# Performance work log

Measured on AMD Instinct MI355X. Metric: run time of the kernel, lower is better.

Reference implementation:

```python
import jax, jax.numpy as jnp
import numpy as np

MAX_CACHE_LEN = 4096


def _rotate_half(t):
    d = t.shape[-1] // 2
    return jnp.concatenate([-t[..., d:], t[..., :d]], axis=-1)


def _apply_rope(t, cos, sin):
    # t: (B, S, H, D); cos/sin: (S, D)
    c = cos[None, :, None, :]
    s = sin[None, :, None, :]
    return t * c + _rotate_half(t) * s


def setup_inputs() -> dict:
    key = jax.random.key(0)
    ks = jax.random.split(key, 7)
    B, S, E, D, KVH = 1, 2048, 2048, 64, 8
    sc = 0.02
    x = jax.random.normal(ks[0], (B, S, E), dtype=jnp.float32)
    Wq = jax.random.normal(ks[1], (E, E), dtype=jnp.float32) * sc
    Wk = jax.random.normal(ks[2], (KVH * D, E), dtype=jnp.float32) * sc
    Wv = jax.random.normal(ks[3], (KVH * D, E), dtype=jnp.float32) * sc
    Wo = jax.random.normal(ks[4], (E, E), dtype=jnp.float32) * sc
    # RoPE tables
    pos = jnp.arange(S, dtype=jnp.float32)[:, None]
    inv_freq = 1.0 / (10000.0 ** (jnp.arange(0, D, 2, dtype=jnp.float32) / D))
    ang = pos * inv_freq[None, :]              # (S, D/2)
    ang = jnp.concatenate([ang, ang], axis=-1)  # (S, D)
    cos = jnp.cos(ang)
    sin = jnp.sin(ang)
    # additive causal mask (1,1,S,S): 0 where allowed, -1e9 where masked
    causal = jnp.tril(jnp.ones((S, S), dtype=bool))
    attn_mask = jnp.where(causal, 0.0, -1e9).astype(jnp.float32)[None, None]
    return {"x": x, "Wq": Wq, "Wk": Wk, "Wv": Wv, "Wo": Wo,
            "cos": cos, "sin": sin, "attn_mask": attn_mask, "last_pos": S}


def reference(x, Wq, Wk, Wv, Wo, cos, sin, attn_mask, last_pos):
    B, S, E = x.shape
    D = cos.shape[-1]
    H = E // D
    KVH = Wk.shape[0] // D
    group = H // KVH

    q = (x @ Wq.T).reshape(B, S, H, D)
    k = (x @ Wk.T).reshape(B, S, KVH, D)
    v = (x @ Wv.T).reshape(B, S, KVH, D)

    q = _apply_rope(q, cos, sin)
    k = _apply_rope(k, cos, sin)

    # KV-cache write (index_copy at positions [last_pos-S, last_pos)), then slice [:last_pos]
    key_cache = jnp.zeros((B, MAX_CACHE_LEN, KVH, D), dtype=x.dtype)
    value_cache = jnp.zeros((B, MAX_CACHE_LEN, KVH, D), dtype=x.dtype)
    key_cache = jax.lax.dynamic_update_slice(key_cache, jax.lax.stop_gradient(k), (0, last_pos - S, 0, 0))
    value_cache = jax.lax.dynamic_update_slice(value_cache, jax.lax.stop_gradient(v), (0, last_pos - S, 0, 0))
    kc = key_cache[:, :last_pos]    # (B, T, KVH, D)
    vc = value_cache[:, :last_pos]

    # GQA: repeat kv heads to match q heads
    kc = jnp.repeat(kc, group, axis=2)  # (B, T, H, D)
    vc = jnp.repeat(vc, group, axis=2)

    scale = 1.0 / np.sqrt(D)
    scores = jnp.einsum('bqhd,bkhd->bhqk', q, kc) * scale
    scores = scores + attn_mask
    probs = jax.nn.softmax(scores.astype(jnp.float32), axis=-1).astype(x.dtype)
    attn = jnp.einsum('bhqk,bkhd->bqhd', probs, vc)  # (B, S, H, D)
    out = attn.reshape(B, S, E) @ Wo.T
    return out
```

## Files before the change

### kernel.cpp

```cpp
#include <hip/hip_runtime.h>
#include <stdint.h>

typedef unsigned short u16;
typedef unsigned int   u32;

typedef __bf16 bf16x8 __attribute__((ext_vector_type(8)));
typedef float  fx4    __attribute__((ext_vector_type(4)));
typedef u16    u16x8  __attribute__((ext_vector_type(8)));
typedef u16    u16x4  __attribute__((ext_vector_type(4)));

typedef __attribute__((address_space(1))) unsigned int as1_u32;
typedef __attribute__((address_space(3))) unsigned int as3_u32;

__device__ __forceinline__ void gload_lds16(const void* g, void* lds) {
  __builtin_amdgcn_global_load_lds((const as1_u32*)(uintptr_t)g,
                                   (as3_u32*)(uintptr_t)lds, 16, 0, 0);
}

__device__ __forceinline__ float b2f(u32 bits) {
  union { u32 i; float f; } v; v.i = bits << 16; return v.f;
}
__device__ __forceinline__ u16 f2b(float f) {
  union { float f; u32 i; } v; v.f = f;
  u32 x = v.i;
  return (u16)((x + 0x7fffu + ((x >> 16) & 1u)) >> 16);
}
__device__ __forceinline__ u16 f2b_hw(float f) {
  union { __bf16 b; u16 u; } v; v.b = (__bf16)f; return v.u;
}

__global__ __launch_bounds__(256) void cast_kernel(
    const float* __restrict__ s0, const float* __restrict__ s1,
    const float* __restrict__ s2, const float* __restrict__ s3,
    const float* __restrict__ s4, u16* __restrict__ dst)
{
  const size_t i8 = ((size_t)blockIdx.x * 256 + threadIdx.x) * 8;
  if (i8 >= 14680064) return;
  const float* src; size_t off;
  if      (i8 <  4194304) { src = s0; off = i8; }
  else if (i8 <  8388608) { src = s1; off = i8 - 4194304; }
  else if (i8 <  9437184) { src = s2; off = i8 - 8388608; }
  else if (i8 < 10485760) { src = s3; off = i8 - 9437184; }
  else                    { src = s4; off = i8 - 10485760; }
  const float4 a = *(const float4*)(src + off);
  const float4 b = *(const float4*)(src + off + 4);
  u16x8 o;
  o[0] = f2b(a.x); o[1] = f2b(a.y); o[2] = f2b(a.z); o[3] = f2b(a.w);
  o[4] = f2b(b.x); o[5] = f2b(b.y); o[6] = f2b(b.z); o[7] = f2b(b.w);
  *(u16x8*)(dst + i8) = o;
}

template <int MODE>
__global__ __launch_bounds__(256) void gemm_bt(
    const u16* __restrict__ A, const u16* __restrict__ B0,
    const u16* __restrict__ B1, const u16* __restrict__ B2,
    void* __restrict__ Cv, int K, int split1, int split2, int ldc,
    const float* __restrict__ cosb, const float* __restrict__ sinb,
    u16* __restrict__ vtg)
{
  __shared__ __align__(16) u16 smem[4 * 8192];

  const int n0 = blockIdx.x * 128;
  const int m0 = blockIdx.y * 128;

  const u16* Bsel; int nb;
  if (n0 < split1)      { Bsel = B0; nb = n0; }
  else if (n0 < split2) { Bsel = B1; nb = n0 - split1; }
  else                  { Bsel = B2; nb = n0 - split2; }

  const int tid  = threadIdx.x;
  const int wave = tid >> 6, lane = tid & 63;
  const int wm = wave >> 1, wn = wave & 1;
  const int quad = lane >> 4, l16 = lane & 15;

  fx4 acc[4][4];
#pragma unroll
  for (int i = 0; i < 4; ++i)
#pragma unroll
    for (int j = 0; j < 4; ++j) acc[i][j] = fx4{0.f, 0.f, 0.f, 0.f};

  const int row = tid >> 2;
  const int cc  = (tid & 3) * 8;
  auto stage = [&](int kt) {
    u16* As = smem + (kt & 3) * 8192;
    u16* Bs = As + 4096;
    const int k0 = kt * 32;
#pragma unroll
    for (int i = 0; i < 2; ++i) {
      const int r2 = row + i * 64;
      const int s  = tid + i * 256;
      gload_lds16(A    + (size_t)(m0 + r2) * K + k0 + cc, As + s * 8);
      gload_lds16(Bsel + (size_t)(nb + r2) * K + k0 + cc, Bs + s * 8);
    }
  };

  const int KT = K >> 5;
  stage(0); stage(1); stage(2);

#pragma unroll 1
  for (int kt = 0; kt < KT; ++kt) {
    const int rem = KT - 1 - kt;
    if (rem >= 3)      asm volatile("s_waitcnt vmcnt(12)\n\ts_barrier" ::: "memory");
    else if (rem == 2) asm volatile("s_waitcnt vmcnt(8)\n\ts_barrier" ::: "memory");
    else if (rem == 1) asm volatile("s_waitcnt vmcnt(4)\n\ts_barrier" ::: "memory");
    else               asm volatile("s_waitcnt vmcnt(0)\n\ts_barrier" ::: "memory");
    if (kt + 3 < KT) stage(kt + 3);

    const u16* As = smem + (kt & 3) * 8192;
    const u16* Bs = As + 4096;

    bf16x8 af[4], bfr[4];
#pragma unroll
    for (int t = 0; t < 4; ++t) {
      af[t]  = *(const bf16x8*)&As[(wm * 64 + t * 16 + l16) * 32 + quad * 8];
      bfr[t] = *(const bf16x8*)&Bs[(wn * 64 + t * 16 + l16) * 32 + quad * 8];
    }
#pragma unroll
    for (int ti = 0; ti < 4; ++ti)
#pragma unroll
      for (int tj = 0; tj < 4; ++tj)
        acc[ti][tj] = __builtin_amdgcn_mfma_f32_16x16x32_bf16(
            af[ti], bfr[tj], acc[ti][tj], 0, 0, 0);
  }

  if (MODE == 1) {
    float* C = (float*)Cv;
#pragma unroll
    for (int ti = 0; ti < 4; ++ti) {
      const int row_b = m0 + wm * 64 + ti * 16 + quad * 4;
#pragma unroll
      for (int tj = 0; tj < 4; ++tj) {
        const int col = n0 + wn * 64 + tj * 16 + l16;
#pragma unroll
        for (int r = 0; r < 4; ++r)
          C[(size_t)(row_b + r) * ldc + col] = acc[ti][tj][r];
      }
    }
  } else {
    u16* C = (u16*)Cv;
    const int cb = n0 + wn * 64;
    if (cb < 2560) {
      const float qs = (cb < 2048) ? 0.125f : 1.0f;
#pragma unroll
      for (int ti = 0; ti < 4; ++ti) {
#pragma unroll
        for (int r = 0; r < 4; ++r) {
          const int s = m0 + wm * 64 + ti * 16 + quad * 4 + r;
          const float* cr = cosb + s * 64;
          const float* sr = sinb + s * 64;
          u16* orow = C + (size_t)s * 3072 + cb;
#pragma unroll
          for (int tj = 0; tj < 2; ++tj) {
            const int d0 = tj * 16 + l16, d1 = d0 + 32;
            const float x0 = acc[ti][tj][r], x1 = acc[ti][tj + 2][r];
            orow[d0] = f2b((x0 * cr[d0] - x1 * sr[d0]) * qs);
            orow[d1] = f2b((x1 * cr[d1] + x0 * sr[d1]) * qs);
          }
        }
      }
    } else {
      const int vr0 = cb - 2560;
#pragma unroll
      for (int ti = 0; ti < 4; ++ti) {
        const int s0 = m0 + wm * 64 + ti * 16 + quad * 4;
#pragma unroll
        for (int tj = 0; tj < 4; ++tj) {
          const int vr = vr0 + tj * 16 + l16;
          u16x4 o;
#pragma unroll
          for (int r = 0; r < 4; ++r) o[r] = f2b(acc[ti][tj][r]);
          *(u16x4*)(vtg + (size_t)vr * 2048 + s0) = o;
        }
      }
    }
  }
}

__global__ __launch_bounds__(256) void attn_kernel(
    const u16* __restrict__ qkv, const u16* __restrict__ vt,
    u16* __restrict__ attnbuf)
{
  const int h   = blockIdx.y;
  const int kvh = h >> 2;
  const int tid = threadIdx.x;
  const int w = tid >> 6, lane = tid & 63;
  const int quad = lane >> 4, l16 = lane & 15;

  __shared__ __align__(16) u16 Qs[64][72];
  __shared__ __align__(16) u16 Ks[128][72];
  __shared__ __align__(16) u16 Vh[2][64][72];
  __shared__ __align__(16) u16 Ps[4][16][72];

  const int kcol = 2048 + kvh * 64;

#pragma unroll 1
  for (int pass = 0; pass < 2; ++pass) {
    const int bx = pass ? (31 - blockIdx.x) : blockIdx.x;
    const int r0 = bx * 64;
    const int nhalf  = bx + 1;
    const int ntiles = (bx + 2) >> 1;

    __syncthreads();

#pragma unroll
    for (int i = 0; i < 2; ++i) {
      const int idx = tid + i * 256;
      const int r = idx >> 3, dc = (idx & 7) * 8;
      *(uint4*)&Qs[r][dc] =
          *(const uint4*)(qkv + (size_t)(r0 + r) * 3072 + h * 64 + dc);
    }

    fx4 O[4];
    float l_r[4];
#pragma unroll
    for (int c = 0; c < 4; ++c) O[c] = fx4{0.f, 0.f, 0.f, 0.f};
#pragma unroll
    for (int r = 0; r < 4; ++r) l_r[r] = 0.f;

#pragma unroll 1
    for (int kt = 0; kt < ntiles; ++kt) {
      const int k0 = kt * 128;
      __syncthreads();
#pragma unroll
      for (int i = 0; i < 4; ++i) {
        const int idx = tid + i * 256;
        const int j = idx >> 3, dc = (idx & 7) * 8;
        *(uint4*)&Ks[j][dc] =
            *(const uint4*)(qkv + (size_t)(k0 + j) * 3072 + kcol + dc);
      }
#pragma unroll
      for (int i = 0; i < 4; ++i) {
        const int idx = tid + i * 256;
        const int hh = idx >> 9, rem = idx & 511;
        const int j = rem >> 3, dc = (rem & 7) * 8;
        *(uint4*)&Vh[hh][j][dc] =
            *(const uint4*)(vt + (size_t)(kvh * 64 + j) * 2048 + k0 + hh * 64 + dc);
      }
      __syncthreads();

      const bf16x8 aq0 = *(const bf16x8*)&Qs[w * 16 + l16][quad * 8];
      const bf16x8 aq1 = *(const bf16x8*)&Qs[w * 16 + l16][32 + quad * 8];

#pragma unroll
      for (int hh = 0; hh < 2; ++hh) {
        const int half = kt * 2 + hh;
        if (half < nhalf) {
          const int k0h = k0 + hh * 64;

          fx4 sc[4];
#pragma unroll
          for (int c = 0; c < 4; ++c) {
            const bf16x8 b0 = *(const bf16x8*)&Ks[hh * 64 + c * 16 + l16][quad * 8];
            const bf16x8 b1 = *(const bf16x8*)&Ks[hh * 64 + c * 16 + l16][32 + quad * 8];
            fx4 z = fx4{0.f, 0.f, 0.f, 0.f};
            z     = __builtin_amdgcn_mfma_f32_16x16x32_bf16(aq0, b0, z, 0, 0, 0);
            sc[c] = __builtin_amdgcn_mfma_f32_16x16x32_bf16(aq1, b1, z, 0, 0, 0);
          }

          if (k0h >= r0) {
#pragma unroll
            for (int c = 0; c < 4; ++c)
#pragma unroll
              for (int r = 0; r < 4; ++r) {
                float p = __expf(sc[c][r]);
                if (k0h + c * 16 + l16 > r0 + w * 16 + quad * 4 + r) p = 0.f;
                l_r[r] += p;
                Ps[w][quad * 4 + r][c * 16 + l16] = f2b_hw(p);
              }
          } else {
#pragma unroll
            for (int c = 0; c < 4; ++c)
#pragma unroll
              for (int r = 0; r < 4; ++r) {
                const float p = __expf(sc[c][r]);
                l_r[r] += p;
                Ps[w][quad * 4 + r][c * 16 + l16] = f2b_hw(p);
              }
          }

          const bf16x8 ap0 = *(const bf16x8*)&Ps[w][l16][quad * 8];
          const bf16x8 ap1 = *(const bf16x8*)&Ps[w][l16][32 + quad * 8];
#pragma unroll
          for (int c = 0; c < 4; ++c) {
            const bf16x8 v0 = *(const bf16x8*)&Vh[hh][c * 16 + l16][quad * 8];
            const bf16x8 v1 = *(const bf16x8*)&Vh[hh][c * 16 + l16][32 + quad * 8];
            O[c] = __builtin_amdgcn_mfma_f32_16x16x32_bf16(ap0, v0, O[c], 0, 0, 0);
            O[c] = __builtin_amdgcn_mfma_f32_16x16x32_bf16(ap1, v1, O[c], 0, 0, 0);
          }
        }
      }
    }

#pragma unroll
    for (int r = 0; r < 4; ++r) {
      float l = l_r[r];
#pragma unroll
      for (int off = 1; off < 16; off <<= 1) l += __shfl_xor(l, off, 64);
      const float inv = 1.f / fmaxf(l, 1e-30f);
      const int qg = r0 + w * 16 + quad * 4 + r;
#pragma unroll
      for (int c = 0; c < 4; ++c)
        attnbuf[(size_t)qg * 2048 + h * 64 + c * 16 + l16] = f2b(O[c][r] * inv);
    }
  }
}

extern "C" void kernel_launch(void* const* d_in, const int* in_sizes, int n_in,
                              void* d_out, int out_size, void* d_ws, size_t ws_size,
                              hipStream_t stream) {
  const float* x    = (const float*)d_in[0];
  const float* Wq   = (const float*)d_in[1];
  const float* Wk   = (const float*)d_in[2];
  const float* Wv   = (const float*)d_in[3];
  const float* Wo   = (const float*)d_in[4];
  const float* cosb = (const float*)d_in[5];
  const float* sinb = (const float*)d_in[6];
  float* out = (float*)d_out;

  u16* ws      = (u16*)d_ws;
  u16* qkv     = ws;
  u16* attnbuf = ws + 6291456;
  u16* xb      = ws + 10485760;
  u16* Wqb     = ws + 14680064;
  u16* Wkb     = ws + 18874368;
  u16* Wvb     = ws + 19922944;
  u16* Wob     = ws + 20971520;
  u16* vtg     = ws + 25165824;

  cast_kernel<<<7168, 256, 0, stream>>>(x, Wq, Wk, Wv, Wo, xb);

  gemm_bt<0><<<dim3(24, 16), 256, 0, stream>>>(
      xb, Wqb, Wkb, Wvb, qkv, 2048, 2048, 2560, 3072, cosb, sinb, vtg);

  attn_kernel<<<dim3(16, 32), 256, 0, stream>>>(qkv, vtg, attnbuf);

  gemm_bt<1><<<dim3(16, 16), 256, 0, stream>>>(
      attnbuf, Wob, Wob, Wob, out, 2048, 1 << 30, 1 << 30, 2048, cosb, sinb, vtg);
}
```

Baseline: 230.6 us.

## Restructure attention into one query tile per block with double-buffered async KV loads

```diff
diff --git a/kernel.cpp b/kernel.cpp
--- a/kernel.cpp
+++ b/kernel.cpp
@@ -180,128 +180,134 @@
     const u16* __restrict__ qkv, const u16* __restrict__ vt,
     u16* __restrict__ attnbuf)
 {
-  const int h   = blockIdx.y;
+  const int h   = blockIdx.x;
   const int kvh = h >> 2;
+  const int bx  = 31 - (int)blockIdx.y;
   const int tid = threadIdx.x;
   const int w = tid >> 6, lane = tid & 63;
   const int quad = lane >> 4, l16 = lane & 15;
 
-  __shared__ __align__(16) u16 Qs[64][72];
-  __shared__ __align__(16) u16 Ks[128][72];
-  __shared__ __align__(16) u16 Vh[2][64][72];
-  __shared__ __align__(16) u16 Ps[4][16][72];
-
-  const int kcol = 2048 + kvh * 64;
+  __shared__ __align__(16) u16 Qs[64 * 64];
+  __shared__ __align__(16) u16 Kb[2][64 * 64];
+  __shared__ __align__(16) u16 Vb[2][64 * 64];
+  __shared__ __align__(16) u16 Ps[4][16 * 64];
+
+  const int r0    = bx * 64;
+  const int nhalf = bx + 1;
+  const int kcol  = 2048 + kvh * 64;
+
+  const int srow = tid >> 3;
+  const int sc   = tid & 7;
+
+  auto stageQ = [&]() {
+#pragma unroll
+    for (int i = 0; i < 2; ++i) {
+      const int r  = srow + i * 32;
+      const int cs = sc ^ (r & 7);
+      gload_lds16(qkv + (size_t)(r0 + r) * 3072 + h * 64 + cs * 8,
+                  Qs + (size_t)(tid + i * 256) * 8);
+    }
+  };
+  auto stageKV = [&](int n) {
+    const int k0 = n * 64;
+    u16* Kd = Kb[n & 1];
+    u16* Vd = Vb[n & 1];
+#pragma unroll
+    for (int i = 0; i < 2; ++i) {
+      const int r  = srow + i * 32;
+      const int cs = sc ^ (r & 7);
+      gload_lds16(qkv + (size_t)(k0 + r) * 3072 + kcol + cs * 8,
+                  Kd + (size_t)(tid + i * 256) * 8);
+      gload_lds16(vt + (size_t)(kvh * 64 + r) * 2048 + k0 + cs * 8,
+                  Vd + (size_t)(tid + i * 256) * 8);
+    }
+  };
+
+  stageQ();
+  stageKV(0);
+  asm volatile("s_waitcnt vmcnt(0)\n\ts_barrier" ::: "memory");
+
+  const int xm = l16 & 7;
+  const int qrow = w * 16 + l16;
+  const bf16x8 aq0 = *(const bf16x8*)&Qs[qrow * 64 + ((quad    ) ^ xm) * 8];
+  const bf16x8 aq1 = *(const bf16x8*)&Qs[qrow * 64 + ((4 + quad) ^ xm) * 8];
+
+  fx4 O[4];
+  float l_r[4];
+#pragma unroll
+  for (int c = 0; c < 4; ++c) O[c] = fx4{0.f, 0.f, 0.f, 0.f};
+#pragma unroll
+  for (int r = 0; r < 4; ++r) l_r[r] = 0.f;
 
 #pragma unroll 1
-  for (int pass = 0; pass < 2; ++pass) {
-    const int bx = pass ? (31 - blockIdx.x) : blockIdx.x;
-    const int r0 = bx * 64;
-    const int nhalf  = bx + 1;
-    const int ntiles = (bx + 2) >> 1;
-
-    __syncthreads();
-
-#pragma unroll
-    for (int i = 0; i < 2; ++i) {
-      const int idx = tid + i * 256;
-      const int r = idx >> 3, dc = (idx & 7) * 8;
-      *(uint4*)&Qs[r][dc] =
-          *(const uint4*)(qkv + (size_t)(r0 + r) * 3072 + h * 64 + dc);
-    }
-
-    fx4 O[4];
-    float l_r[4];
-#pragma unroll
-    for (int c = 0; c < 4; ++c) O[c] = fx4{0.f, 0.f, 0.f, 0.f};
-#pragma unroll
-    for (int r = 0; r < 4; ++r) l_r[r] = 0.f;
-
-#pragma unroll 1
-    for (int kt = 0; kt < ntiles; ++kt) {
-      const int k0 = kt * 128;
-      __syncthreads();
-#pragma unroll
-      for (int i = 0; i < 4; ++i) {
-        const int idx = tid + i * 256;
-        const int j = idx >> 3, dc = (idx & 7) * 8;
-        *(uint4*)&Ks[j][dc] =
-            *(const uint4*)(qkv + (size_t)(k0 + j) * 3072 + kcol + dc);
-      }
-#pragma unroll
-      for (int i = 0; i < 4; ++i) {
-        const int idx = tid + i * 256;
-        const int hh = idx >> 9, rem = idx & 511;
-        const int j = rem >> 3, dc = (rem & 7) * 8;
-        *(uint4*)&Vh[hh][j][dc] =
-            *(const uint4*)(vt + (size_t)(kvh * 64 + j) * 2048 + k0 + hh * 64 + dc);
-      }
-      __syncthreads();
-
-      const bf16x8 aq0 = *(const bf16x8*)&Qs[w * 16 + l16][quad * 8];
-      const bf16x8 aq1 = *(const bf16x8*)&Qs[w * 16 + l16][32 + quad * 8];
-
-#pragma unroll
-      for (int hh = 0; hh < 2; ++hh) {
-        const int half = kt * 2 + hh;
-        if (half < nhalf) {
-          const int k0h = k0 + hh * 64;
-
-          fx4 sc[4];
-#pragma unroll
-          for (int c = 0; c < 4; ++c) {
-            const bf16x8 b0 = *(const bf16x8*)&Ks[hh * 64 + c * 16 + l16][quad * 8];
-            const bf16x8 b1 = *(const bf16x8*)&Ks[hh * 64 + c * 16 + l16][32 + quad * 8];
-            fx4 z = fx4{0.f, 0.f, 0.f, 0.f};
-            z     = __builtin_amdgcn_mfma_f32_16x16x32_bf16(aq0, b0, z, 0, 0, 0);
-            sc[c] = __builtin_amdgcn_mfma_f32_16x16x32_bf16(aq1, b1, z, 0, 0, 0);
-          }
-
-          if (k0h >= r0) {
-#pragma unroll
-            for (int c = 0; c < 4; ++c)
-#pragma unroll
-              for (int r = 0; r < 4; ++r) {
-                float p = __expf(sc[c][r]);
-                if (k0h + c * 16 + l16 > r0 + w * 16 + quad * 4 + r) p = 0.f;
-                l_r[r] += p;
-                Ps[w][quad * 4 + r][c * 16 + l16] = f2b_hw(p);
-              }
-          } else {
-#pragma unroll
-            for (int c = 0; c < 4; ++c)
-#pragma unroll
-              for (int r = 0; r < 4; ++r) {
-                const float p = __expf(sc[c][r]);
-                l_r[r] += p;
-                Ps[w][quad * 4 + r][c * 16 + l16] = f2b_hw(p);
-              }
-          }
-
-          const bf16x8 ap0 = *(const bf16x8*)&Ps[w][l16][quad * 8];
-          const bf16x8 ap1 = *(const bf16x8*)&Ps[w][l16][32 + quad * 8];
-#pragma unroll
-          for (int c = 0; c < 4; ++c) {
-            const bf16x8 v0 = *(const bf16x8*)&Vh[hh][c * 16 + l16][quad * 8];
-            const bf16x8 v1 = *(const bf16x8*)&Vh[hh][c * 16 + l16][32 + quad * 8];
-            O[c] = __builtin_amdgcn_mfma_f32_16x16x32_bf16(ap0, v0, O[c], 0, 0, 0);
-            O[c] = __builtin_amdgcn_mfma_f32_16x16x32_bf16(ap1, v1, O[c], 0, 0, 0);
-          }
+  for (int n = 0; n < nhalf; ++n) {
+    if (n + 1 < nhalf) stageKV(n + 1);
+    const u16* Kh = Kb[n & 1];
+    const u16* Vd = Vb[n & 1];
+    const int k0h = n * 64;
+
+    fx4 sc4[4];
+    __builtin_amdgcn_s_setprio(1);
+#pragma unroll
+    for (int c = 0; c < 4; ++c) {
+      const int kr = c * 16 + l16;
+      const bf16x8 b0 = *(const bf16x8*)&Kh[kr * 64 + ((quad    ) ^ xm) * 8];
+      const bf16x8 b1 = *(const bf16x8*)&Kh[kr * 64 + ((4 + quad) ^ xm) * 8];
+      fx4 z = fx4{0.f, 0.f, 0.f, 0.f};
+      z      = __builtin_amdgcn_mfma_f32_16x16x32_bf16(aq0, b0, z, 0, 0, 0);
+      sc4[c] = __builtin_amdgcn_mfma_f32_16x16x32_bf16(aq1, b1, z, 0, 0, 0);
+    }
+    __builtin_amdgcn_s_setprio(0);
+
+    if (k0h >= r0) {
+#pragma unroll
+      for (int c = 0; c < 4; ++c)
+#pragma unroll
+        for (int r = 0; r < 4; ++r) {
+          float p = __expf(sc4[c][r]);
+          if (k0h + c * 16 + l16 > r0 + w * 16 + quad * 4 + r) p = 0.f;
+          l_r[r] += p;
+          const int pr = quad * 4 + r;
+          Ps[w][pr * 64 + ((c * 16 + l16) ^ ((pr & 7) << 3))] = f2b_hw(p);
         }
-      }
-    }
-
-#pragma unroll
-    for (int r = 0; r < 4; ++r) {
-      float l = l_r[r];
-#pragma unroll
-      for (int off = 1; off < 16; off <<= 1) l += __shfl_xor(l, off, 64);
-      const float inv = 1.f / fmaxf(l, 1e-30f);
-      const int qg = r0 + w * 16 + quad * 4 + r;
+    } else {
 #pragma unroll
       for (int c = 0; c < 4; ++c)
-        attnbuf[(size_t)qg * 2048 + h * 64 + c * 16 + l16] = f2b(O[c][r] * inv);
-    }
+#pragma unroll
+        for (int r = 0; r < 4; ++r) {
+          const float p = __expf(sc4[c][r]);
+          l_r[r] += p;
+          const int pr = quad * 4 + r;
+          Ps[w][pr * 64 + ((c * 16 + l16) ^ ((pr & 7) << 3))] = f2b_hw(p);
+        }
+    }
+
+    const bf16x8 ap0 = *(const bf16x8*)&Ps[w][l16 * 64 + ((quad    ) ^ xm) * 8];
+    const bf16x8 ap1 = *(const bf16x8*)&Ps[w][l16 * 64 + ((4 + quad) ^ xm) * 8];
+    __builtin_amdgcn_s_setprio(1);
+#pragma unroll
+    for (int c = 0; c < 4; ++c) {
+      const int vr = c * 16 + l16;
+      const bf16x8 v0 = *(const bf16x8*)&Vd[vr * 64 + ((quad    ) ^ xm) * 8];
+      const bf16x8 v1 = *(const bf16x8*)&Vd[vr * 64 + ((4 + quad) ^ xm) * 8];
+      O[c] = __builtin_amdgcn_mfma_f32_16x16x32_bf16(ap0, v0, O[c], 0, 0, 0);
+      O[c] = __builtin_amdgcn_mfma_f32_16x16x32_bf16(ap1, v1, O[c], 0, 0, 0);
+    }
+    __builtin_amdgcn_s_setprio(0);
+
+    asm volatile("s_waitcnt vmcnt(0)\n\ts_barrier" ::: "memory");
+  }
+
+#pragma unroll
+  for (int r = 0; r < 4; ++r) {
+    float l = l_r[r];
+#pragma unroll
+    for (int off = 1; off < 16; off <<= 1) l += __shfl_xor(l, off, 64);
+    const float inv = 1.f / fmaxf(l, 1e-30f);
+    const int qg = r0 + w * 16 + quad * 4 + r;
+#pragma unroll
+    for (int c = 0; c < 4; ++c)
+      attnbuf[(size_t)qg * 2048 + h * 64 + c * 16 + l16] = f2b(O[c][r] * inv);
   }
 }
 
@@ -332,7 +338,7 @@
   gemm_bt<0><<<dim3(24, 16), 256, 0, stream>>>(
       xb, Wqb, Wkb, Wvb, qkv, 2048, 2048, 2560, 3072, cosb, sinb, vtg);
 
-  attn_kernel<<<dim3(16, 32), 256, 0, stream>>>(qkv, vtg, attnbuf);
+  attn_kernel<<<dim3(32, 32), 256, 0, stream>>>(qkv, vtg, attnbuf);
 
   gemm_bt<1><<<dim3(16, 16), 256, 0, stream>>>(
       attnbuf, Wob, Wob, Wob, out, 2048, 1 << 30, 1 << 30, 2048, cosb, sinb, vtg);
```

Result: faster. 223.6 us (-3.0%).
